# Performance work log

Hardware: AMD Instinct MI355X
Metric: run time of the kernel (lower is better)

## Reference

```python
import jax, jax.numpy as jnp
import numpy as np


def _relative_position_index(w):
    # Deterministic Swin relative-position index, shape [w*w, w*w], values in [0, (2w-1)^2)
    coords_h = np.arange(w)
    coords_w = np.arange(w)
    coords = np.stack(np.meshgrid(coords_h, coords_w, indexing="ij"))  # [2, w, w]
    coords = coords.reshape(2, -1)                                      # [2, w*w]
    rel = coords[:, :, None] - coords[:, None, :]                       # [2, N, N]
    rel = rel.transpose(1, 2, 0).copy()                                 # [N, N, 2]
    rel[:, :, 0] += w - 1
    rel[:, :, 1] += w - 1
    rel[:, :, 0] *= 2 * w - 1
    return jnp.asarray(rel.sum(-1), dtype=jnp.int32)


def setup_inputs() -> dict:
    key = jax.random.key(0)
    ks = jax.random.split(key, 7)
    BS, N, C, H, W = 4096, 49, 384, 12, 7
    NW = 64  # number of windows per image
    x = jax.random.normal(ks[0], (BS, N, C), dtype=jnp.float32)
    # Swin shift mask: 0 where attention allowed, -100 where blocked
    u = jax.random.uniform(ks[1], (NW, N, N))
    mask = jnp.where(u < 0.5, 0.0, -100.0).astype(jnp.float32)
    qkv_w = jax.random.normal(ks[2], (C, 3 * C), dtype=jnp.float32) * (C ** -0.5)
    qkv_b = jax.random.normal(ks[3], (3 * C,), dtype=jnp.float32) * 0.02
    proj_w = jax.random.normal(ks[4], (C, C), dtype=jnp.float32) * (C ** -0.5)
    proj_b = jax.random.normal(ks[5], (C,), dtype=jnp.float32) * 0.02
    bias_table = jax.random.normal(ks[6], ((2 * W - 1) ** 2, H), dtype=jnp.float32) * 0.02
    return {"x": x, "mask": mask, "qkv_w": qkv_w, "qkv_b": qkv_b,
            "proj_w": proj_w, "proj_b": proj_b, "bias_table": bias_table,
            "n_heads": 12, "window_size": 7}


def reference(x, mask, qkv_w, qkv_b, proj_w, proj_b, bias_table, n_heads, window_size):
    BS, N, C = x.shape
    Hh = n_heads
    hd = C // Hh
    scale = hd ** -0.5
    rpi = _relative_position_index(window_size)  # [N, N] int

    qkv = x @ qkv_w + qkv_b                       # [BS, N, 3C]
    qkv = qkv.reshape(BS, N, 3, Hh, hd).transpose(2, 0, 3, 1, 4)  # [3, BS, H, N, hd]
    q, k, v = qkv[0], qkv[1], qkv[2]

    attn = jnp.einsum("bhnd,bhmd->bhnm", q, k) * scale   # [BS, H, N, N]
    # relative position bias gather: [N*N, H] -> [H, N, N]
    rpb = bias_table[rpi.reshape(-1)].reshape(N, N, Hh).transpose(2, 0, 1)
    attn = attn + rpb[None]

    nw = mask.shape[0]
    attn = attn.reshape(BS // nw, nw, Hh, N, N) + mask[None, :, None]
    attn = attn.reshape(BS, Hh, N, N)

    attn = jax.nn.softmax(attn, axis=-1)
    out = jnp.einsum("bhnm,bhmd->bhnd", attn, v)          # [BS, H, N, hd]
    out = out.transpose(0, 2, 1, 3).reshape(BS, N, C)
    return out @ proj_w + proj_b
```

## Files before the change

kernel.cpp:

```cpp
#include <hip/hip_runtime.h>
#include <hip/hip_bf16.h>


typedef __attribute__((ext_vector_type(8))) short bf16x8;
typedef __attribute__((ext_vector_type(4))) float f32x4;

#define SEQ_N  49
#define CH     384
#define QKV_N  1152
#define UNIT_ROWS 3136
#define BM2_ELEMS (64 * 12 * 49 * 64)

__device__ __forceinline__ unsigned short f2b(float f) {
    union { float f; unsigned int u; } v; v.f = f;
    return (unsigned short)((v.u + 0x7FFFu + ((v.u >> 16) & 1u)) >> 16);
}

__device__ __forceinline__ bf16x8 ld8(const unsigned short* p) {
    return *(const bf16x8*)p;
}

__device__ __forceinline__ void gload16(const unsigned short* g, unsigned short* l) {
    __builtin_amdgcn_global_load_lds(
        (const __attribute__((address_space(1))) unsigned int*)g,
        (__attribute__((address_space(3))) unsigned int*)l, 16, 0, 0);
}

__device__ __forceinline__ int xcd_swizzle(int orig, int T) {
    int q = T >> 3, r = T & 7;
    int xcd = orig & 7, idx = orig >> 3;
    return (xcd < r ? xcd * (q + 1) : r * (q + 1) + (xcd - r) * q) + idx;
}

__global__ __launch_bounds__(256) void k_cvt_w(const float* __restrict__ wq,
        const float* __restrict__ wp, unsigned short* __restrict__ oq,
        unsigned short* __restrict__ op)
{
    int t = blockIdx.x * 256 + threadIdx.x;
    if (t < QKV_N * CH) {
        int n = t / CH, k = t - n * CH;
        oq[t] = f2b(wq[(size_t)k * QKV_N + n]);
    }
    if (t < CH * CH) {
        int n = t / CH, k = t - n * CH;
        op[t] = f2b(wp[(size_t)k * CH + n]);
    }
}

__global__ __launch_bounds__(256) void k_bm(const float* __restrict__ btab,
        const float* __restrict__ mask, float* __restrict__ bm2)
{
    int t = blockIdx.x * 256 + threadIdx.x;
    if (t >= BM2_ELEMS) return;
    int w    = t / (12 * 49 * 64);
    int rem  = t - w * 12 * 49 * 64;
    int h    = rem / (49 * 64);
    int rem2 = rem - h * 49 * 64;
    int i    = rem2 >> 6;
    int s    = rem2 & 63;
    int j15  = s >> 2, nt = s & 3;
    int j    = nt * 16 + j15;
    float v = -1e30f;
    if (j < 49) {
        int ih = i / 7, iw = i - (i / 7) * 7;
        int jh = j / 7, jw = j - (j / 7) * 7;
        int idx = (ih - jh + 6) * 13 + (iw - jw + 6);
        v = btab[idx * 12 + h] + mask[(size_t)w * 2401 + i * 49 + j];
    }
    bm2[t] = v;
}

__global__ __launch_bounds__(256) void k_cvt(const float* __restrict__ in,
        unsigned short* __restrict__ outp, int n8)
{
    int stride = gridDim.x * 256;
    for (int i = blockIdx.x * 256 + threadIdx.x; i < n8; i += stride) {
        const float4* p = (const float4*)(in + (size_t)i * 8);
        float4 a = p[0], b = p[1];
        uint4 v;
        v.x = (unsigned)f2b(a.x) | ((unsigned)f2b(a.y) << 16);
        v.y = (unsigned)f2b(a.z) | ((unsigned)f2b(a.w) << 16);
        v.z = (unsigned)f2b(b.x) | ((unsigned)f2b(b.y) << 16);
        v.w = (unsigned)f2b(b.z) | ((unsigned)f2b(b.w) << 16);
        *(uint4*)(outp + (size_t)i * 8) = v;
    }
}

template<int OUTF32>
__global__ __launch_bounds__(512, 6) void k_gemm(
        const unsigned short* __restrict__ A, int lda,
        const unsigned short* __restrict__ Bt, int K,
        const float* __restrict__ bias,
        unsigned short* __restrict__ Cb, float* __restrict__ Cf, int ldc,
        int M, int ntiles, int mtiles)
{
    __shared__ unsigned short As[3 * 4096];
    __shared__ unsigned short Bs[3 * 4096];
    const int wg = xcd_swizzle(blockIdx.x, mtiles * ntiles);
    const int m0 = (wg / ntiles) * 128;
    const int n0 = (wg % ntiles) * 128;
    const int tid = threadIdx.x;
    const int lane = tid & 63, wv = tid >> 6;
    const int wr = wv >> 2, wc = wv & 3;
    const int l15 = lane & 15, g = lane >> 4;

    f32x4 acc[4][2];
#pragma unroll
    for (int a = 0; a < 4; ++a)
#pragma unroll
        for (int b = 0; b < 2; ++b) acc[a][b] = (f32x4){0.f, 0.f, 0.f, 0.f};

    int arow = m0 + (tid >> 2); if (arow > M - 1) arow = M - 1;
    const unsigned short* aP = A + (size_t)arow * lda + (tid & 3) * 8;
    const unsigned short* bP = Bt + (size_t)(n0 + (tid >> 2)) * K + (tid & 3) * 8;
    const int lo = wv * 512;

#define STAGE(kt, buf) do {                                \
        gload16(aP + (kt), &As[(buf) * 4096 + lo]);        \
        gload16(bP + (kt), &Bs[(buf) * 4096 + lo]);        \
    } while (0)

#define COMPUTE(buf) do {                                                       \
        bf16x8 af[4], bfr[2];                                                   \
        _Pragma("unroll")                                                       \
        for (int mt = 0; mt < 4; ++mt)                                          \
            af[mt] = ld8(&As[(buf) * 4096 + (wr * 64 + mt * 16 + l15) * 32 + g * 8]); \
        _Pragma("unroll")                                                       \
        for (int nt = 0; nt < 2; ++nt)                                          \
            bfr[nt] = ld8(&Bs[(buf) * 4096 + (wc * 32 + nt * 16 + l15) * 32 + g * 8]); \
        __builtin_amdgcn_s_setprio(1);                                          \
        _Pragma("unroll")                                                       \
        for (int mt = 0; mt < 4; ++mt)                                          \
            _Pragma("unroll")                                                   \
            for (int nt = 0; nt < 2; ++nt)                                      \
                acc[mt][nt] = __builtin_amdgcn_mfma_f32_16x16x32_bf16(          \
                        af[mt], bfr[nt], acc[mt][nt], 0, 0, 0);                 \
        __builtin_amdgcn_s_setprio(0);                                          \
    } while (0)

    const int nsteps = K >> 5;

    STAGE(0, 0);
    STAGE(32, 1);

    for (int t = 0; t < nsteps; ++t) {
        if (t + 1 < nsteps) asm volatile("s_waitcnt vmcnt(2)" ::: "memory");
        else                asm volatile("s_waitcnt vmcnt(0)" ::: "memory");
        __builtin_amdgcn_sched_barrier(0);
        __builtin_amdgcn_s_barrier();
        __builtin_amdgcn_sched_barrier(0);
        if (t + 2 < nsteps) {
            int pf = t + 2; pf -= (pf / 3) * 3;
            STAGE((t + 2) * 32, pf);
        }
        COMPUTE(t - (t / 3) * 3);
    }
#undef STAGE
#undef COMPUTE

#pragma unroll
    for (int mt = 0; mt < 4; ++mt)
#pragma unroll
        for (int nt = 0; nt < 2; ++nt) {
            int col = n0 + wc * 32 + nt * 16 + l15;
            float bb = bias[col];
#pragma unroll
            for (int r = 0; r < 4; ++r) {
                int row = m0 + wr * 64 + mt * 16 + g * 4 + r;
                if (row < M) {
                    if (OUTF32)
                        Cf[(size_t)row * ldc + col] = acc[mt][nt][r] + bb;
                    else
                        Cb[(size_t)row * ldc + col] = f2b(acc[mt][nt][r] + bb);
                }
            }
        }
}

__global__ __launch_bounds__(256) void k_attn(unsigned short* __restrict__ qkv,
        const float* __restrict__ bm2)
{
    extern __shared__ unsigned short sm[];
    const int tid = threadIdx.x;
    const int lane = tid & 63, wv = tid >> 6;
    const int l15 = lane & 15, g = lane >> 4;
    const int pair = blockIdx.x * 4 + wv;
    const int winloc = pair / 12;
    const int h = pair - winloc * 12;
    const int wimg = winloc & 63;
    const int co = h * 32;
    unsigned short* Vt = sm + wv * 5056;
    unsigned short* Pw = Vt + 2304;
    unsigned short* src = qkv + (size_t)winloc * SEQ_N * QKV_N;
    const float* bm2h = bm2 + ((size_t)(wimg * 12 + h)) * (49 * 64);

    for (int t = lane; t < 32 * 16; t += 64) {
        int c = t >> 4, kk = 48 + (t & 15);
        Vt[c * 72 + kk] = 0;
    }
    for (int t = lane; t < 49 * 4; t += 64) {
        int row = t >> 2, cb = (t & 3) * 8;
        const unsigned short* vp = src + (size_t)row * QKV_N + 768 + co + cb;
        ushort4 a = ((const ushort4*)vp)[0];
        ushort4 b = ((const ushort4*)vp)[1];
        Vt[(cb + 0) * 72 + row] = a.x; Vt[(cb + 1) * 72 + row] = a.y;
        Vt[(cb + 2) * 72 + row] = a.z; Vt[(cb + 3) * 72 + row] = a.w;
        Vt[(cb + 4) * 72 + row] = b.x; Vt[(cb + 5) * 72 + row] = b.y;
        Vt[(cb + 6) * 72 + row] = b.z; Vt[(cb + 7) * 72 + row] = b.w;
    }

    bf16x8 qf[4], kf[4];
#pragma unroll
    for (int mt = 0; mt < 4; ++mt) {
        int r = mt * 16 + l15; if (r > 48) r = 48;
        qf[mt] = ld8(src + (size_t)r * QKV_N + co + g * 8);
    }
#pragma unroll
    for (int nt = 0; nt < 4; ++nt) {
        int r = nt * 16 + l15; if (r > 48) r = 48;
        kf[nt] = ld8(src + (size_t)r * QKV_N + CH + co + g * 8);
    }

    f32x4 sa[4][4];
#pragma unroll
    for (int mt = 0; mt < 4; ++mt)
#pragma unroll
        for (int nt = 0; nt < 4; ++nt) sa[mt][nt] = (f32x4){0.f, 0.f, 0.f, 0.f};
#pragma unroll
    for (int mt = 0; mt < 4; ++mt)
#pragma unroll
        for (int nt = 0; nt < 4; ++nt)
            sa[mt][nt] = __builtin_amdgcn_mfma_f32_16x16x32_bf16(
                    qf[mt], kf[nt], sa[mt][nt], 0, 0, 0);

    const float scale = 0.17677669529663687f;
#pragma unroll
    for (int mt = 0; mt < 4; ++mt) {
#pragma unroll
        for (int r = 0; r < 4; ++r) {
            int i = mt * 16 + g * 4 + r;
            int ic = i < 49 ? i : 48;
            float4 bv = *(const float4*)(bm2h + (size_t)ic * 64 + l15 * 4);
            float sv[4];
            sv[0] = sa[mt][0][r] * scale + bv.x;
            sv[1] = sa[mt][1][r] * scale + bv.y;
            sv[2] = sa[mt][2][r] * scale + bv.z;
            sv[3] = sa[mt][3][r] * scale + bv.w;
            float mx = fmaxf(fmaxf(sv[0], sv[1]), fmaxf(sv[2], sv[3]));
#pragma unroll
            for (int d = 1; d < 16; d <<= 1) mx = fmaxf(mx, __shfl_xor(mx, d));
            float sum = 0.f;
#pragma unroll
            for (int nt = 0; nt < 4; ++nt) { sv[nt] = __expf(sv[nt] - mx); sum += sv[nt]; }
#pragma unroll
            for (int d = 1; d < 16; d <<= 1) sum += __shfl_xor(sum, d);
            float inv = 1.0f / sum;
            if (i < 49) {
#pragma unroll
                for (int nt = 0; nt < 4; ++nt) {
                    int j = nt * 16 + l15;
                    if (j < 56) Pw[i * 56 + j] = f2b(sv[nt] * inv);
                }
            }
        }
    }

    f32x4 oa[4][2];
#pragma unroll
    for (int mt = 0; mt < 4; ++mt)
#pragma unroll
        for (int nt = 0; nt < 2; ++nt) oa[mt][nt] = (f32x4){0.f, 0.f, 0.f, 0.f};
#pragma unroll
    for (int ks = 0; ks < 2; ++ks) {
        bf16x8 pf[4];
#pragma unroll
        for (int mt = 0; mt < 4; ++mt) {
            int pr = mt * 16 + l15; if (pr > 48) pr = 48;
            pf[mt] = ld8(Pw + pr * 56 + ks * 32 + g * 8);
        }
#pragma unroll
        for (int nt = 0; nt < 2; ++nt) {
            bf16x8 vf = ld8(Vt + (nt * 16 + l15) * 72 + ks * 32 + g * 8);
#pragma unroll
            for (int mt = 0; mt < 4; ++mt)
                oa[mt][nt] = __builtin_amdgcn_mfma_f32_16x16x32_bf16(
                        pf[mt], vf, oa[mt][nt], 0, 0, 0);
        }
    }

#pragma unroll
    for (int mt = 0; mt < 4; ++mt)
#pragma unroll
        for (int r = 0; r < 4; ++r) {
            int i = mt * 16 + g * 4 + r;
            if (i < 49) {
#pragma unroll
                for (int nt = 0; nt < 2; ++nt)
                    src[(size_t)i * QKV_N + co + nt * 16 + l15] = f2b(oa[mt][nt][r]);
            }
        }
}

extern "C" void kernel_launch(void* const* d_in, const int* in_sizes, int n_in,
                              void* d_out, int out_size, void* d_ws, size_t ws_size,
                              hipStream_t stream) {
    const float* x      = (const float*)d_in[0];
    const float* mask   = (const float*)d_in[1];
    const float* qkv_w  = (const float*)d_in[2];
    const float* qkv_b  = (const float*)d_in[3];
    const float* proj_w = (const float*)d_in[4];
    const float* proj_b = (const float*)d_in[5];
    const float* btab   = (const float*)d_in[6];
    float* out = (float*)d_out;

    unsigned short* wq_bt = (unsigned short*)d_ws;
    unsigned short* wp_bt = wq_bt + QKV_N * CH;
    float*          bm2   = (float*)(wp_bt + CH * CH);
    unsigned short* base  = (unsigned short*)(bm2 + BM2_ELEMS);
    const size_t fixed = (size_t)(QKV_N * CH + CH * CH) * 2 + (size_t)BM2_ELEMS * 4;
    const size_t unit  = (size_t)UNIT_ROWS * (CH + QKV_N) * 2;
    if (ws_size < fixed + unit) return;
    int upc = (int)((ws_size - fixed) / unit);
    if (upc > 64) upc = 64;
    unsigned short* xb  = base;
    unsigned short* qkv = base + (size_t)upc * UNIT_ROWS * CH;

    const int smem2 = 4 * 5056 * 2;
    hipFuncSetAttribute(reinterpret_cast<const void*>(k_attn),
                        hipFuncAttributeMaxDynamicSharedMemorySize, smem2);

    dim3 blk(256);
    k_cvt_w<<<dim3((QKV_N * CH + 255) / 256), blk, 0, stream>>>(qkv_w, proj_w, wq_bt, wp_bt);
    k_bm   <<<dim3((BM2_ELEMS + 255) / 256), blk, 0, stream>>>(btab, mask, bm2);

    for (int u0 = 0; u0 < 64; u0 += upc) {
        int units = (64 - u0) < upc ? (64 - u0) : upc;
        int m_base = u0 * UNIT_ROWS;
        int Mc = units * UNIT_ROWS;
        int mtiles = (Mc + 127) / 128;
        k_cvt<<<dim3(2048), blk, 0, stream>>>(x + (size_t)m_base * CH, xb, Mc * 48);
        k_gemm<0><<<dim3(mtiles * 9), dim3(512), 0, stream>>>(
                xb, CH, wq_bt, CH, qkv_b, qkv, nullptr, QKV_N, Mc, 9, mtiles);
        k_attn<<<dim3(units * 192), blk, smem2, stream>>>(qkv, bm2);
        k_gemm<1><<<dim3(mtiles * 3), dim3(512), 0, stream>>>(
                qkv, QKV_N, wp_bt, CH, proj_b, nullptr, out + (size_t)m_base * CH,
                CH, Mc, 3, mtiles);
    }
}
```

Baseline: 860.6 us.

## Fuse window attention with output projection in one per-window kernel

Each block now handles a whole window: its four waves loop over three heads each, write the attention output into LDS, and after a barrier compute the 384x384 output projection directly from LDS, reading the bf16 weights from global memory. This removes the separate projection GEMM launch and the round trip of attention output through the qkv buffer in global memory. In exchange, every block re-reads the full projection weight matrix (cached in L2), grid parallelism drops by a factor of three, LDS use per block grows, and the small per-window projection (49 rows padded to 64) may use the MFMA units less efficiently than the tiled GEMM.

```diff
diff --git a/kernel.cpp b/kernel.cpp
--- a/kernel.cpp
+++ b/kernel.cpp
@@ -10,6 +10,7 @@
 #define QKV_N  1152
 #define UNIT_ROWS 3136
 #define BM2_ELEMS (64 * 12 * 49 * 64)
+#define OLDS_STRIDE 392
 
 __device__ __forceinline__ unsigned short f2b(float f) {
     union { float f; unsigned int u; } v; v.f = f;
@@ -177,126 +178,174 @@
         }
 }
 
-__global__ __launch_bounds__(256) void k_attn(unsigned short* __restrict__ qkv,
-        const float* __restrict__ bm2)
+__global__ __launch_bounds__(256) void k_attnp(
+        const unsigned short* __restrict__ qkv,
+        const float* __restrict__ bm2,
+        const unsigned short* __restrict__ wp_bt,
+        const float* __restrict__ proj_b,
+        float* __restrict__ out, int win_base_rows)
 {
     extern __shared__ unsigned short sm[];
     const int tid = threadIdx.x;
     const int lane = tid & 63, wv = tid >> 6;
     const int l15 = lane & 15, g = lane >> 4;
-    const int pair = blockIdx.x * 4 + wv;
-    const int winloc = pair / 12;
-    const int h = pair - winloc * 12;
+    const int winloc = blockIdx.x;
     const int wimg = winloc & 63;
-    const int co = h * 32;
-    unsigned short* Vt = sm + wv * 5056;
+    unsigned short* O_lds = sm;
+    unsigned short* Vt = sm + SEQ_N * OLDS_STRIDE + wv * 5056;
     unsigned short* Pw = Vt + 2304;
-    unsigned short* src = qkv + (size_t)winloc * SEQ_N * QKV_N;
-    const float* bm2h = bm2 + ((size_t)(wimg * 12 + h)) * (49 * 64);
-
-    for (int t = lane; t < 32 * 16; t += 64) {
-        int c = t >> 4, kk = 48 + (t & 15);
-        Vt[c * 72 + kk] = 0;
-    }
-    for (int t = lane; t < 49 * 4; t += 64) {
-        int row = t >> 2, cb = (t & 3) * 8;
-        const unsigned short* vp = src + (size_t)row * QKV_N + 768 + co + cb;
-        ushort4 a = ((const ushort4*)vp)[0];
-        ushort4 b = ((const ushort4*)vp)[1];
-        Vt[(cb + 0) * 72 + row] = a.x; Vt[(cb + 1) * 72 + row] = a.y;
-        Vt[(cb + 2) * 72 + row] = a.z; Vt[(cb + 3) * 72 + row] = a.w;
-        Vt[(cb + 4) * 72 + row] = b.x; Vt[(cb + 5) * 72 + row] = b.y;
-        Vt[(cb + 6) * 72 + row] = b.z; Vt[(cb + 7) * 72 + row] = b.w;
-    }
-
-    bf16x8 qf[4], kf[4];
-#pragma unroll
-    for (int mt = 0; mt < 4; ++mt) {
-        int r = mt * 16 + l15; if (r > 48) r = 48;
-        qf[mt] = ld8(src + (size_t)r * QKV_N + co + g * 8);
-    }
-#pragma unroll
-    for (int nt = 0; nt < 4; ++nt) {
-        int r = nt * 16 + l15; if (r > 48) r = 48;
-        kf[nt] = ld8(src + (size_t)r * QKV_N + CH + co + g * 8);
-    }
-
-    f32x4 sa[4][4];
-#pragma unroll
-    for (int mt = 0; mt < 4; ++mt)
-#pragma unroll
-        for (int nt = 0; nt < 4; ++nt) sa[mt][nt] = (f32x4){0.f, 0.f, 0.f, 0.f};
-#pragma unroll
-    for (int mt = 0; mt < 4; ++mt)
-#pragma unroll
-        for (int nt = 0; nt < 4; ++nt)
-            sa[mt][nt] = __builtin_amdgcn_mfma_f32_16x16x32_bf16(
-                    qf[mt], kf[nt], sa[mt][nt], 0, 0, 0);
-
-    const float scale = 0.17677669529663687f;
-#pragma unroll
-    for (int mt = 0; mt < 4; ++mt) {
-#pragma unroll
-        for (int r = 0; r < 4; ++r) {
-            int i = mt * 16 + g * 4 + r;
-            int ic = i < 49 ? i : 48;
-            float4 bv = *(const float4*)(bm2h + (size_t)ic * 64 + l15 * 4);
-            float sv[4];
-            sv[0] = sa[mt][0][r] * scale + bv.x;
-            sv[1] = sa[mt][1][r] * scale + bv.y;
-            sv[2] = sa[mt][2][r] * scale + bv.z;
-            sv[3] = sa[mt][3][r] * scale + bv.w;
-            float mx = fmaxf(fmaxf(sv[0], sv[1]), fmaxf(sv[2], sv[3]));
-#pragma unroll
-            for (int d = 1; d < 16; d <<= 1) mx = fmaxf(mx, __shfl_xor(mx, d));
-            float sum = 0.f;
-#pragma unroll
-            for (int nt = 0; nt < 4; ++nt) { sv[nt] = __expf(sv[nt] - mx); sum += sv[nt]; }
-#pragma unroll
-            for (int d = 1; d < 16; d <<= 1) sum += __shfl_xor(sum, d);
-            float inv = 1.0f / sum;
-            if (i < 49) {
-#pragma unroll
-                for (int nt = 0; nt < 4; ++nt) {
-                    int j = nt * 16 + l15;
-                    if (j < 56) Pw[i * 56 + j] = f2b(sv[nt] * inv);
+    const unsigned short* src = qkv + (size_t)winloc * SEQ_N * QKV_N;
+
+    for (int hi = 0; hi < 3; ++hi) {
+        const int h = wv + hi * 4;
+        const int co = h * 32;
+        const float* bm2h = bm2 + ((size_t)(wimg * 12 + h)) * (49 * 64);
+
+        for (int t = lane; t < 32 * 16; t += 64) {
+            int c = t >> 4, kk = 48 + (t & 15);
+            Vt[c * 72 + kk] = 0;
+        }
+        for (int t = lane; t < 49 * 4; t += 64) {
+            int row = t >> 2, cb = (t & 3) * 8;
+            const unsigned short* vp = src + (size_t)row * QKV_N + 768 + co + cb;
+            ushort4 a = ((const ushort4*)vp)[0];
+            ushort4 b = ((const ushort4*)vp)[1];
+            Vt[(cb + 0) * 72 + row] = a.x; Vt[(cb + 1) * 72 + row] = a.y;
+            Vt[(cb + 2) * 72 + row] = a.z; Vt[(cb + 3) * 72 + row] = a.w;
+            Vt[(cb + 4) * 72 + row] = b.x; Vt[(cb + 5) * 72 + row] = b.y;
+            Vt[(cb + 6) * 72 + row] = b.z; Vt[(cb + 7) * 72 + row] = b.w;
+        }
+
+        bf16x8 qf[4], kf[4];
+#pragma unroll
+        for (int mt = 0; mt < 4; ++mt) {
+            int r = mt * 16 + l15; if (r > 48) r = 48;
+            qf[mt] = ld8(src + (size_t)r * QKV_N + co + g * 8);
+        }
+#pragma unroll
+        for (int nt = 0; nt < 4; ++nt) {
+            int r = nt * 16 + l15; if (r > 48) r = 48;
+            kf[nt] = ld8(src + (size_t)r * QKV_N + CH + co + g * 8);
+        }
+
+        f32x4 sa[4][4];
+#pragma unroll
+        for (int mt = 0; mt < 4; ++mt)
+#pragma unroll
+            for (int nt = 0; nt < 4; ++nt) sa[mt][nt] = (f32x4){0.f, 0.f, 0.f, 0.f};
+#pragma unroll
+        for (int mt = 0; mt < 4; ++mt)
+#pragma unroll
+            for (int nt = 0; nt < 4; ++nt)
+                sa[mt][nt] = __builtin_amdgcn_mfma_f32_16x16x32_bf16(
+                        qf[mt], kf[nt], sa[mt][nt], 0, 0, 0);
+
+        const float scale = 0.17677669529663687f;
+#pragma unroll
+        for (int mt = 0; mt < 4; ++mt) {
+#pragma unroll
+            for (int r = 0; r < 4; ++r) {
+                int i = mt * 16 + g * 4 + r;
+                int ic = i < 49 ? i : 48;
+                float4 bv = *(const float4*)(bm2h + (size_t)ic * 64 + l15 * 4);
+                float sv[4];
+                sv[0] = sa[mt][0][r] * scale + bv.x;
+                sv[1] = sa[mt][1][r] * scale + bv.y;
+                sv[2] = sa[mt][2][r] * scale + bv.z;
+                sv[3] = sa[mt][3][r] * scale + bv.w;
+                float mx = fmaxf(fmaxf(sv[0], sv[1]), fmaxf(sv[2], sv[3]));
+#pragma unroll
+                for (int d = 1; d < 16; d <<= 1) mx = fmaxf(mx, __shfl_xor(mx, d));
+                float sum = 0.f;
+#pragma unroll
+                for (int nt = 0; nt < 4; ++nt) { sv[nt] = __expf(sv[nt] - mx); sum += sv[nt]; }
+#pragma unroll
+                for (int d = 1; d < 16; d <<= 1) sum += __shfl_xor(sum, d);
+                float inv = 1.0f / sum;
+                if (i < 49) {
+#pragma unroll
+                    for (int nt = 0; nt < 4; ++nt) {
+                        int j = nt * 16 + l15;
+                        if (j < 56) Pw[i * 56 + j] = f2b(sv[nt] * inv);
+                    }
                 }
             }
         }
-    }
-
-    f32x4 oa[4][2];
-#pragma unroll
-    for (int mt = 0; mt < 4; ++mt)
-#pragma unroll
-        for (int nt = 0; nt < 2; ++nt) oa[mt][nt] = (f32x4){0.f, 0.f, 0.f, 0.f};
-#pragma unroll
-    for (int ks = 0; ks < 2; ++ks) {
-        bf16x8 pf[4];
+
+        f32x4 oa[4][2];
+#pragma unroll
+        for (int mt = 0; mt < 4; ++mt)
+#pragma unroll
+            for (int nt = 0; nt < 2; ++nt) oa[mt][nt] = (f32x4){0.f, 0.f, 0.f, 0.f};
+#pragma unroll
+        for (int ks = 0; ks < 2; ++ks) {
+            bf16x8 pf[4];
+#pragma unroll
+            for (int mt = 0; mt < 4; ++mt) {
+                int pr = mt * 16 + l15; if (pr > 48) pr = 48;
+                pf[mt] = ld8(Pw + pr * 56 + ks * 32 + g * 8);
+            }
+#pragma unroll
+            for (int nt = 0; nt < 2; ++nt) {
+                bf16x8 vf = ld8(Vt + (nt * 16 + l15) * 72 + ks * 32 + g * 8);
+#pragma unroll
+                for (int mt = 0; mt < 4; ++mt)
+                    oa[mt][nt] = __builtin_amdgcn_mfma_f32_16x16x32_bf16(
+                            pf[mt], vf, oa[mt][nt], 0, 0, 0);
+            }
+        }
+
+#pragma unroll
+        for (int mt = 0; mt < 4; ++mt)
+#pragma unroll
+            for (int r = 0; r < 4; ++r) {
+                int i = mt * 16 + g * 4 + r;
+                if (i < 49) {
+#pragma unroll
+                    for (int nt = 0; nt < 2; ++nt)
+                        O_lds[i * OLDS_STRIDE + co + nt * 16 + l15] = f2b(oa[mt][nt][r]);
+                }
+            }
+    }
+
+    __syncthreads();
+
+    f32x4 pacc[4][6];
+#pragma unroll
+    for (int a = 0; a < 4; ++a)
+#pragma unroll
+        for (int b = 0; b < 6; ++b) pacc[a][b] = (f32x4){0.f, 0.f, 0.f, 0.f};
+
+    for (int ks = 0; ks < 12; ++ks) {
+        bf16x8 paf[4];
 #pragma unroll
         for (int mt = 0; mt < 4; ++mt) {
             int pr = mt * 16 + l15; if (pr > 48) pr = 48;
-            pf[mt] = ld8(Pw + pr * 56 + ks * 32 + g * 8);
-        }
-#pragma unroll
-        for (int nt = 0; nt < 2; ++nt) {
-            bf16x8 vf = ld8(Vt + (nt * 16 + l15) * 72 + ks * 32 + g * 8);
+            paf[mt] = ld8(&O_lds[pr * OLDS_STRIDE + ks * 32 + g * 8]);
+        }
+#pragma unroll
+        for (int nt = 0; nt < 6; ++nt) {
+            bf16x8 pbf = ld8(wp_bt +
+                (size_t)(wv * 96 + nt * 16 + l15) * CH + ks * 32 + g * 8);
 #pragma unroll
             for (int mt = 0; mt < 4; ++mt)
-                oa[mt][nt] = __builtin_amdgcn_mfma_f32_16x16x32_bf16(
-                        pf[mt], vf, oa[mt][nt], 0, 0, 0);
+                pacc[mt][nt] = __builtin_amdgcn_mfma_f32_16x16x32_bf16(
+                        paf[mt], pbf, pacc[mt][nt], 0, 0, 0);
         }
     }
 
 #pragma unroll
     for (int mt = 0; mt < 4; ++mt)
 #pragma unroll
-        for (int r = 0; r < 4; ++r) {
-            int i = mt * 16 + g * 4 + r;
-            if (i < 49) {
-#pragma unroll
-                for (int nt = 0; nt < 2; ++nt)
-                    src[(size_t)i * QKV_N + co + nt * 16 + l15] = f2b(oa[mt][nt][r]);
+        for (int nt = 0; nt < 6; ++nt) {
+            int col = wv * 96 + nt * 16 + l15;
+            float bb = proj_b[col];
+#pragma unroll
+            for (int r = 0; r < 4; ++r) {
+                int row = mt * 16 + g * 4 + r;
+                if (row < SEQ_N)
+                    out[(size_t)(win_base_rows + winloc * SEQ_N + row) * CH + col]
+                        = pacc[mt][nt][r] + bb;
             }
         }
 }
@@ -325,9 +374,9 @@
     unsigned short* xb  = base;
     unsigned short* qkv = base + (size_t)upc * UNIT_ROWS * CH;
 
-    const int smem2 = 4 * 5056 * 2;
-    hipFuncSetAttribute(reinterpret_cast<const void*>(k_attn),
-                        hipFuncAttributeMaxDynamicSharedMemorySize, smem2);
+    const int smemA = (SEQ_N * OLDS_STRIDE + 4 * 5056) * 2;
+    hipFuncSetAttribute(reinterpret_cast<const void*>(k_attnp),
+                        hipFuncAttributeMaxDynamicSharedMemorySize, smemA);
 
     dim3 blk(256);
     k_cvt_w<<<dim3((QKV_N * CH + 255) / 256), blk, 0, stream>>>(qkv_w, proj_w, wq_bt, wp_bt);
@@ -341,9 +390,7 @@
         k_cvt<<<dim3(2048), blk, 0, stream>>>(x + (size_t)m_base * CH, xb, Mc * 48);
         k_gemm<0><<<dim3(mtiles * 9), dim3(512), 0, stream>>>(
                 xb, CH, wq_bt, CH, qkv_b, qkv, nullptr, QKV_N, Mc, 9, mtiles);
-        k_attn<<<dim3(units * 192), blk, smem2, stream>>>(qkv, bm2);
-        k_gemm<1><<<dim3(mtiles * 3), dim3(512), 0, stream>>>(
-                qkv, QKV_N, wp_bt, CH, proj_b, nullptr, out + (size_t)m_base * CH,
-                CH, Mc, 3, mtiles);
-    }
-}
+        k_attnp<<<dim3(units * 64), blk, smemA, stream>>>(
+                qkv, bm2, wp_bt, proj_b, out, m_base);
+    }
+}
```

Measured after the change: 1.363 ms. +58.3%, slower.
